# Kernel tuning notes

Hardware: AMD Instinct MI355X
Metric: run time of the kernel (lower is better)

## Reference

```python
import jax, jax.numpy as jnp
import numpy as np
import math

BATCH, LEN, HID, STATE = 16, 4096, 512, 128
DT_MIN, DT_MAX = 1e-3, 0.1
STEP_RESCALE = 1.0
CONJ_SYM = True


def setup_inputs() -> dict:
    key = jax.random.key(0)
    ks = jax.random.split(key, 7)
    inputs = jax.random.normal(ks[0], (BATCH, LEN, HID), jnp.float32)
    # stable continuous-time eigenvalues: negative real part
    lambda_real = -0.5 * jnp.abs(jax.random.normal(ks[1], (STATE,), jnp.float32)) - 1e-3
    lambda_imag = jnp.pi * jax.random.normal(ks[2], (STATE,), jnp.float32)
    B = jax.random.normal(ks[3], (STATE, HID, 2), jnp.float32) * (1.0 / math.sqrt(HID))
    C = jax.random.normal(ks[4], (HID, STATE, 2), jnp.float32) * (1.0 / math.sqrt(STATE))
    D = jax.random.normal(ks[5], (HID,), jnp.float32)
    u = jax.random.uniform(ks[6], (STATE, 1), jnp.float32)
    log_step = u * (math.log(DT_MAX) - math.log(DT_MIN)) + math.log(DT_MIN)
    return dict(inputs=inputs, lambda_real=lambda_real, lambda_imag=lambda_imag,
                B=B, C=C, D=D, log_step=log_step)


def _s5_forward(inputs, lambda_real, lambda_imag, B, C, D, log_step):
    # complex diagonal state matrix (P,)
    lam = (lambda_real + 1j * lambda_imag).astype(jnp.complex64)
    step = STEP_RESCALE * jnp.exp(log_step[:, 0])          # (P,)
    lambda_bar = jnp.exp(lam * step.astype(jnp.complex64))  # ZOH discretization, (P,)
    B_c = (B[..., 0] + 1j * B[..., 1]).astype(jnp.complex64)  # (P, H)
    C_c = (C[..., 0] + 1j * C[..., 1]).astype(jnp.complex64)  # (H, P)
    # ZOH input matrix: B_bar = (lambda_bar - 1) / lambda * B
    b_bar = ((lambda_bar - 1.0) / lam)[:, None] * B_c          # (P, H)
    # per-timestep driving term: (L, B, P)
    bu = jnp.einsum('blh,ph->lbp', inputs.astype(jnp.complex64), b_bar)
    L = inputs.shape[1]
    a = jnp.broadcast_to(lambda_bar[None, None, :], (L, 1, STATE))  # constant decay per step

    def combine(e1, e2):
        a1, b1 = e1
        a2, b2 = e2
        return (a2 * a1, a2 * b1 + b2)

    # parallel (Blelchoch-style) scan of x_t = lambda_bar * x_{t-1} + bu_t
    _, states = jax.lax.associative_scan(combine, (a, bu))      # states: (L, B, P)
    y = jnp.einsum('lbp,hp->blh', states, C_c)                  # (B, L, H) complex
    out = 2.0 * y.real if CONJ_SYM else y.real
    return out + D * inputs


def reference(inputs, lambda_real, lambda_imag, B, C, D, log_step):
    return _s5_forward(inputs, lambda_real, lambda_imag, B, C, D, log_step)
```

## Files before the change

### kernel.cpp

```cpp
#include <hip/hip_runtime.h>
#include <math.h>

#define B_   16
#define L_   4096
#define H_   512
#define P_   128
#define M_   (B_*L_)
#define N2_  (2*P_)

typedef __attribute__((ext_vector_type(8))) short bf16x8;
typedef __attribute__((ext_vector_type(8))) unsigned short u16x8;
typedef __attribute__((ext_vector_type(4))) float f32x4;

__device__ __forceinline__ unsigned short f2bf(float x) {
    unsigned u = __float_as_uint(x);
    return (unsigned short)((u + 0x7FFFu + ((u >> 16) & 1u)) >> 16);
}
__device__ __forceinline__ float bf2f(unsigned short s) {
    return __uint_as_float(((unsigned)s) << 16);
}

__device__ __forceinline__ void gload16(const void* g, void* l) {
    __builtin_amdgcn_global_load_lds(
        (const __attribute__((address_space(1))) void*)g,
        (__attribute__((address_space(3))) void*)l,
        16, 0, 0);
}


__global__ void precompA(const float* __restrict__ lr, const float* __restrict__ li,
                         const float* __restrict__ lstep,
                         float* __restrict__ abar_r, float* __restrict__ abar_i,
                         float* __restrict__ coef_r, float* __restrict__ coef_i) {
    int p = threadIdx.x;
    if (p >= P_) return;
    double lrd = (double)lr[p], lid = (double)li[p];
    double step = exp((double)lstep[p]);
    double ea = exp(lrd * step);
    double abr = ea * cos(lid * step), abi = ea * sin(lid * step);
    abar_r[p] = (float)abr; abar_i[p] = (float)abi;
    double nr = abr - 1.0, ni = abi;
    double den = lrd*lrd + lid*lid;
    coef_r[p] = (float)((nr*lrd + ni*lid) / den);
    coef_i[p] = (float)((ni*lrd - nr*lid) / den);
}

__global__ void precompBT(const float* __restrict__ Bin,
                          const float* __restrict__ coef_r, const float* __restrict__ coef_i,
                          unsigned short* __restrict__ BTh) {
    int idx = blockIdx.x * 256 + threadIdx.x;
    if (idx >= N2_*H_) return;
    int n = idx >> 9, k = idx & 511;
    int p = n & (P_-1);
    float br = Bin[(p*H_ + k)*2 + 0], bi = Bin[(p*H_ + k)*2 + 1];
    float cr = coef_r[p], ci = coef_i[p];
    float v = (n < P_) ? (cr*br - ci*bi) : (cr*bi + ci*br);
    BTh[idx] = f2bf(v);
}

__global__ void precompCM(const float* __restrict__ Cin,
                          unsigned short* __restrict__ CMh) {
    int idx = blockIdx.x * 256 + threadIdx.x;
    if (idx >= H_*N2_) return;
    int n = idx >> 8, k = idx & 255;
    float v;
    if (k < P_) v =  2.0f * Cin[(n*P_ + k)*2 + 0];
    else        v = -2.0f * Cin[(n*P_ + (k-P_))*2 + 1];
    CMh[idx] = f2bf(v);
}


template<int KSTEPS>
__global__ __launch_bounds__(256) void gemm1f(
        const float* __restrict__ A,
        const unsigned short* __restrict__ Bm,
        unsigned short* __restrict__ bu) {
    constexpr int K = KSTEPS * 32;
    __shared__ float Asf[128 * 32];
    __shared__ unsigned short Bs[128 * 32];

    int t = threadIdx.x;
    int nx = gridDim.x;
    int flat = blockIdx.x + nx * blockIdx.y;
    int per  = (nx * gridDim.y) >> 3;
    int nid  = (flat & 7) * per + (flat >> 3);
    int n0 = (nid & (nx - 1)) * 128;
    int m0 = (nid / nx) * 128;

    int lane = t & 63;
    int w    = t >> 6;
    int wr = w >> 1, wc = w & 1;
    int lr = lane & 15, lg = lane >> 4;

    int arow = t >> 3, ach = t & 7;
    int asw  = ach ^ (arow & 7);
    const float* gA = A + (size_t)(m0 + arow) * K + asw * 4;
    int brow = t >> 2, bch = t & 3;
    const unsigned short* gB = Bm + (size_t)(n0 + brow) * K + bch * 8;
    int bbase = w * 512;

    f32x4 acc[4][4] = {};

    for (int ks = 0; ks < KSTEPS; ++ks) {
        int k0 = ks * 32;
        __syncthreads();
#pragma unroll
        for (int i = 0; i < 4; ++i)
            gload16(gA + (size_t)(32 * i) * K + k0, &Asf[i * 1024 + w * 256]);
        gload16(gB + k0,                   &Bs[bbase]);
        gload16(gB + (size_t)64 * K + k0,  &Bs[2048 + bbase]);
        __syncthreads();

        bf16x8 af[4], bf[4];
#pragma unroll
        for (int f = 0; f < 4; ++f) {
            int rA = wr * 64 + f * 16 + lr;
            int c0 = ((2 * lg) ^ (rA & 7)) * 4;
            int c1 = ((2 * lg + 1) ^ (rA & 7)) * 4;
            float4 a0 = *(const float4*)&Asf[rA * 32 + c0];
            float4 a1 = *(const float4*)&Asf[rA * 32 + c1];
            u16x8 h;
            h[0] = f2bf(a0.x); h[1] = f2bf(a0.y); h[2] = f2bf(a0.z); h[3] = f2bf(a0.w);
            h[4] = f2bf(a1.x); h[5] = f2bf(a1.y); h[6] = f2bf(a1.z); h[7] = f2bf(a1.w);
            af[f] = *(bf16x8*)&h;
            int rB = wc * 64 + f * 16 + lr;
            bf[f] = *(const bf16x8*)&Bs[rB * 32 + lg * 8];
        }
#pragma unroll
        for (int fn = 0; fn < 4; ++fn)
#pragma unroll
            for (int fm = 0; fm < 4; ++fm)
                acc[fn][fm] = __builtin_amdgcn_mfma_f32_16x16x32_bf16(bf[fn], af[fm], acc[fn][fm], 0, 0, 0);
    }

#pragma unroll
    for (int fn = 0; fn < 4; ++fn)
#pragma unroll
        for (int fm = 0; fm < 4; ++fm) {
            int m = m0 + wr * 64 + fm * 16 + lr;
            int n = n0 + wc * 64 + fn * 16 + lg * 4;
            ushort4 o;
            o.x = f2bf(acc[fn][fm][0]); o.y = f2bf(acc[fn][fm][1]);
            o.z = f2bf(acc[fn][fm][2]); o.w = f2bf(acc[fn][fm][3]);
            *(ushort4*)&bu[(size_t)m * N2_ + n] = o;
        }
}


template<int KSTEPS, bool HASD>
__global__ __launch_bounds__(256) void gemm_m97(
        const unsigned short* __restrict__ A,
        const unsigned short* __restrict__ Bm,
        float* __restrict__ Cout, int N,
        const float* __restrict__ Din, const float* __restrict__ Dv) {
    constexpr int K = KSTEPS * 32;
    __shared__ unsigned short As[128 * 32];
    __shared__ unsigned short Bs[128 * 32];

    int t = threadIdx.x;
    int nx = gridDim.x;
    int flat = blockIdx.x + nx * blockIdx.y;
    int per  = (nx * gridDim.y) >> 3;
    int nid  = (flat & 7) * per + (flat >> 3);
    int n0 = (nid & (nx - 1)) * 128;
    int m0 = (nid / nx) * 128;

    int lane = t & 63;
    int w    = t >> 6;
    int wr = w >> 1, wc = w & 1;
    int lr = lane & 15, lg = lane >> 4;

    int srow = t >> 2;
    int sq   = t & 3;
    const unsigned short* gA = A  + (size_t)(m0 + srow) * K + sq * 8;
    const unsigned short* gB = Bm + (size_t)(n0 + srow) * K + sq * 8;
    int ldsb = w * 512;

    f32x4 acc[4][4] = {};

    for (int ks = 0; ks < KSTEPS; ++ks) {
        int k0 = ks * 32;
        __syncthreads();
        gload16(gA + k0,                  As + ldsb);
        gload16(gA + (size_t)64 * K + k0, As + 2048 + ldsb);
        gload16(gB + k0,                  Bs + ldsb);
        gload16(gB + (size_t)64 * K + k0, Bs + 2048 + ldsb);
        __syncthreads();

        bf16x8 af[4], bf[4];
#pragma unroll
        for (int f = 0; f < 4; ++f) {
            af[f] = *(const bf16x8*)&As[(wr * 64 + f * 16 + lr) * 32 + lg * 8];
            bf[f] = *(const bf16x8*)&Bs[(wc * 64 + f * 16 + lr) * 32 + lg * 8];
        }
#pragma unroll
        for (int fn = 0; fn < 4; ++fn)
#pragma unroll
            for (int fm = 0; fm < 4; ++fm)
                acc[fn][fm] = __builtin_amdgcn_mfma_f32_16x16x32_bf16(bf[fn], af[fm], acc[fn][fm], 0, 0, 0);
    }

#pragma unroll
    for (int fn = 0; fn < 4; ++fn)
#pragma unroll
        for (int fm = 0; fm < 4; ++fm) {
            int m = m0 + wr * 64 + fm * 16 + lr;
            int n = n0 + wc * 64 + fn * 16 + lg * 4;
            float4 v = make_float4(acc[fn][fm][0], acc[fn][fm][1], acc[fn][fm][2], acc[fn][fm][3]);
            if (HASD) {
                float4 di = *(const float4*)&Din[(size_t)m * N + n];
                float4 dv = *(const float4*)&Dv[n];
                v.x += dv.x * di.x; v.y += dv.y * di.y;
                v.z += dv.z * di.z; v.w += dv.w * di.w;
            }
            *(float4*)&Cout[(size_t)m * N + n] = v;
        }
}


__global__ __launch_bounds__(256) void scan_carry(const unsigned short* __restrict__ bu,
        const float* __restrict__ ar_, const float* __restrict__ ai_,
        float* __restrict__ carr) {
    __shared__ float lds[64][256];
    int t = threadIdx.x;
    int c = blockIdx.x, b = blockIdx.y;
    size_t base = ((size_t)(b*L_ + c*256)) * N2_;
    float ar = 0.f, ai = 0.f, xr = 0.f, xi = 0.f;
    if (t < 128) { ar = ar_[t]; ai = ai_[t]; }
    for (int s = 0; s < 4; s++) {
        __syncthreads();
        const unsigned short* g = bu + base + (size_t)s * 64 * N2_;
#pragma unroll
        for (int it = 0; it < 8; it++) {
            int flat = it * 2048 + t * 8;
            u16x8 v = *(const u16x8*)&g[flat];
            float4 x0 = make_float4(bf2f(v[0]), bf2f(v[1]), bf2f(v[2]), bf2f(v[3]));
            float4 x1 = make_float4(bf2f(v[4]), bf2f(v[5]), bf2f(v[6]), bf2f(v[7]));
            *(float4*)&lds[0][flat]     = x0;
            *(float4*)&lds[0][flat + 4] = x1;
        }
        __syncthreads();
        if (t < 128) {
            for (int i = 0; i < 64; i++) {
                float br = lds[i][t], bi = lds[i][t + 128];
                float nr = ar*xr - ai*xi + br;
                float ni = ar*xi + ai*xr + bi;
                xr = nr; xi = ni;
            }
        }
    }
    if (t < 128) {
        size_t o = ((size_t)(b*16 + c)) * N2_;
        carr[o + t] = xr; carr[o + t + 128] = xi;
    }
}

__global__ void scan_chunks(const float* __restrict__ carr, float* __restrict__ pre,
                            const float* __restrict__ ar_, const float* __restrict__ ai_) {
    int id = blockIdx.x * 256 + threadIdx.x;
    if (id >= B_ * P_) return;
    int b = id >> 7, p = id & (P_-1);
    float mr = ar_[p], mi = ai_[p];
#pragma unroll
    for (int s = 0; s < 8; s++) { float tr = mr*mr - mi*mi; mi = 2.f*mr*mi; mr = tr; }
    float xr = 0.f, xi = 0.f;
    for (int c = 0; c < 16; c++) {
        size_t o = ((size_t)(b*16 + c)) * N2_;
        pre[o + p] = xr; pre[o + p + 128] = xi;
        float cr = carr[o + p], ci = carr[o + p + 128];
        float nr = mr*xr - mi*xi + cr;
        float ni = mr*xi + mi*xr + ci;
        xr = nr; xi = ni;
    }
}

__global__ __launch_bounds__(256) void scan_apply(const unsigned short* __restrict__ bu,
        const float* __restrict__ ar_, const float* __restrict__ ai_,
        const float* __restrict__ pre, unsigned short* __restrict__ states_h) {
    __shared__ float lds[64][256];
    int t = threadIdx.x;
    int c = blockIdx.x, b = blockIdx.y;
    size_t base = ((size_t)(b*L_ + c*256)) * N2_;
    float ar = 0.f, ai = 0.f, xr = 0.f, xi = 0.f;
    if (t < 128) {
        ar = ar_[t]; ai = ai_[t];
        size_t o = ((size_t)(b*16 + c)) * N2_;
        xr = pre[o + t]; xi = pre[o + t + 128];
    }
    for (int s = 0; s < 4; s++) {
        __syncthreads();
        const unsigned short* g = bu + base + (size_t)s * 64 * N2_;
#pragma unroll
        for (int it = 0; it < 8; it++) {
            int flat = it * 2048 + t * 8;
            u16x8 v = *(const u16x8*)&g[flat];
            float4 x0 = make_float4(bf2f(v[0]), bf2f(v[1]), bf2f(v[2]), bf2f(v[3]));
            float4 x1 = make_float4(bf2f(v[4]), bf2f(v[5]), bf2f(v[6]), bf2f(v[7]));
            *(float4*)&lds[0][flat]     = x0;
            *(float4*)&lds[0][flat + 4] = x1;
        }
        __syncthreads();
        if (t < 128) {
            for (int i = 0; i < 64; i++) {
                float br = lds[i][t], bi = lds[i][t + 128];
                float nr = ar*xr - ai*xi + br;
                float ni = ar*xi + ai*xr + bi;
                xr = nr; xi = ni;
                lds[i][t] = xr; lds[i][t + 128] = xi;
            }
        }
        __syncthreads();
        unsigned short* o = states_h + base + (size_t)s * 64 * N2_;
#pragma unroll
        for (int it = 0; it < 8; it++) {
            int flat = it * 2048 + t * 8;
            float4 v0 = *(const float4*)&lds[0][flat];
            float4 v1 = *(const float4*)&lds[0][flat + 4];
            u16x8 ov;
            ov[0] = f2bf(v0.x); ov[1] = f2bf(v0.y); ov[2] = f2bf(v0.z); ov[3] = f2bf(v0.w);
            ov[4] = f2bf(v1.x); ov[5] = f2bf(v1.y); ov[6] = f2bf(v1.z); ov[7] = f2bf(v1.w);
            *(u16x8*)&o[flat] = ov;
        }
    }
}


extern "C" void kernel_launch(void* const* d_in, const int* in_sizes, int n_in,
                              void* d_out, int out_size, void* d_ws, size_t ws_size,
                              hipStream_t stream) {
    const float* inputs = (const float*)d_in[0];
    const float* lr     = (const float*)d_in[1];
    const float* li     = (const float*)d_in[2];
    const float* Bin    = (const float*)d_in[3];
    const float* Cin    = (const float*)d_in[4];
    const float* Dv     = (const float*)d_in[5];
    const float* lstep  = (const float*)d_in[6];
    float* out = (float*)d_out;

    unsigned short* bu = (unsigned short*)d_out;

    float* ws     = (float*)d_ws;
    float* abar_r = ws;
    float* abar_i = ws + 128;
    float* coef_r = ws + 256;
    float* coef_i = ws + 384;
    float* carr   = ws + 512;
    float* pre    = ws + 66048;
    unsigned short* BTh = (unsigned short*)(ws + 131584);
    unsigned short* CMh = BTh + N2_*H_;
    unsigned short* states_h = CMh + H_*N2_;

    hipLaunchKernelGGL(precompA, dim3(1), dim3(128), 0, stream,
                       lr, li, lstep, abar_r, abar_i, coef_r, coef_i);
    hipLaunchKernelGGL(precompBT, dim3((N2_*H_)/256), dim3(256), 0, stream,
                       Bin, coef_r, coef_i, BTh);
    hipLaunchKernelGGL(precompCM, dim3((H_*N2_)/256), dim3(256), 0, stream,
                       Cin, CMh);
    hipLaunchKernelGGL((gemm1f<16>), dim3(N2_/128, M_/128), dim3(256), 0, stream,
                       inputs, BTh, bu);
    hipLaunchKernelGGL(scan_carry, dim3(16, B_), dim3(256), 0, stream,
                       bu, abar_r, abar_i, carr);
    hipLaunchKernelGGL(scan_chunks, dim3(8), dim3(256), 0, stream,
                       carr, pre, abar_r, abar_i);
    hipLaunchKernelGGL(scan_apply, dim3(16, B_), dim3(256), 0, stream,
                       bu, abar_r, abar_i, pre, states_h);
    hipLaunchKernelGGL((gemm_m97<8, true>), dim3(H_/128, M_/128), dim3(256), 0, stream,
                       states_h, CMh, out, H_, inputs, Dv);
}
```

Baseline: 155.1 us.

## Triple-buffer LDS tiles with async prefetch in both GEMM kernels

Both GEMM kernels now use three LDS buffers and prefetch tiles two K-steps ahead with global_load_lds. Each step waits only on the current tile via vmcnt and a single barrier, where before it used two __syncthreads per step. The goal is to overlap global-to-LDS loads with MFMA compute and to raise wave priority during the MFMA block. This triples LDS use per block, which may lower occupancy, and the hand-set vmcnt counts depend on the exact number of loads per stage.

```diff
diff --git a/kernel.cpp b/kernel.cpp
--- a/kernel.cpp
+++ b/kernel.cpp
@@ -76,8 +76,8 @@
         const unsigned short* __restrict__ Bm,
         unsigned short* __restrict__ bu) {
     constexpr int K = KSTEPS * 32;
-    __shared__ float Asf[128 * 32];
-    __shared__ unsigned short Bs[128 * 32];
+    __shared__ float Asf[3][128 * 32];
+    __shared__ unsigned short Bs[3][128 * 32];
 
     int t = threadIdx.x;
     int nx = gridDim.x;
@@ -101,15 +101,33 @@
 
     f32x4 acc[4][4] = {};
 
+#define STAGE1(BUF, KS0)                                                     \
+    {                                                                        \
+        int k0_ = (KS0) * 32;                                                \
+        _Pragma("unroll")                                                    \
+        for (int i = 0; i < 4; ++i)                                          \
+            gload16(gA + (size_t)(32 * i) * K + k0_,                         \
+                    &Asf[BUF][i * 1024 + w * 256]);                          \
+        gload16(gB + k0_,                  &Bs[BUF][bbase]);                 \
+        gload16(gB + (size_t)64 * K + k0_, &Bs[BUF][2048 + bbase]);          \
+    }
+
+    STAGE1(0, 0);
+    STAGE1(1, 1);
+
+#pragma unroll
     for (int ks = 0; ks < KSTEPS; ++ks) {
-        int k0 = ks * 32;
-        __syncthreads();
-#pragma unroll
-        for (int i = 0; i < 4; ++i)
-            gload16(gA + (size_t)(32 * i) * K + k0, &Asf[i * 1024 + w * 256]);
-        gload16(gB + k0,                   &Bs[bbase]);
-        gload16(gB + (size_t)64 * K + k0,  &Bs[2048 + bbase]);
-        __syncthreads();
+        int cur = ks % 3;
+        if (ks + 1 < KSTEPS) {
+            asm volatile("s_waitcnt vmcnt(6)" ::: "memory");
+        } else {
+            asm volatile("s_waitcnt vmcnt(0)" ::: "memory");
+        }
+        __builtin_amdgcn_sched_barrier(0);
+        __builtin_amdgcn_s_barrier();
+        __builtin_amdgcn_sched_barrier(0);
+        if (ks + 2 < KSTEPS)
+            STAGE1((ks + 2) % 3, ks + 2);
 
         bf16x8 af[4], bf[4];
 #pragma unroll
@@ -117,21 +135,24 @@
             int rA = wr * 64 + f * 16 + lr;
             int c0 = ((2 * lg) ^ (rA & 7)) * 4;
             int c1 = ((2 * lg + 1) ^ (rA & 7)) * 4;
-            float4 a0 = *(const float4*)&Asf[rA * 32 + c0];
-            float4 a1 = *(const float4*)&Asf[rA * 32 + c1];
+            float4 a0 = *(const float4*)&Asf[cur][rA * 32 + c0];
+            float4 a1 = *(const float4*)&Asf[cur][rA * 32 + c1];
             u16x8 h;
             h[0] = f2bf(a0.x); h[1] = f2bf(a0.y); h[2] = f2bf(a0.z); h[3] = f2bf(a0.w);
             h[4] = f2bf(a1.x); h[5] = f2bf(a1.y); h[6] = f2bf(a1.z); h[7] = f2bf(a1.w);
             af[f] = *(bf16x8*)&h;
             int rB = wc * 64 + f * 16 + lr;
-            bf[f] = *(const bf16x8*)&Bs[rB * 32 + lg * 8];
-        }
+            bf[f] = *(const bf16x8*)&Bs[cur][rB * 32 + lg * 8];
+        }
+        __builtin_amdgcn_s_setprio(1);
 #pragma unroll
         for (int fn = 0; fn < 4; ++fn)
 #pragma unroll
             for (int fm = 0; fm < 4; ++fm)
                 acc[fn][fm] = __builtin_amdgcn_mfma_f32_16x16x32_bf16(bf[fn], af[fm], acc[fn][fm], 0, 0, 0);
-    }
+        __builtin_amdgcn_s_setprio(0);
+    }
+#undef STAGE1
 
 #pragma unroll
     for (int fn = 0; fn < 4; ++fn)
@@ -154,8 +175,8 @@
         float* __restrict__ Cout, int N,
         const float* __restrict__ Din, const float* __restrict__ Dv) {
     constexpr int K = KSTEPS * 32;
-    __shared__ unsigned short As[128 * 32];
-    __shared__ unsigned short Bs[128 * 32];
+    __shared__ unsigned short As[3][128 * 32];
+    __shared__ unsigned short Bs[3][128 * 32];
 
     int t = threadIdx.x;
     int nx = gridDim.x;
@@ -178,27 +199,47 @@
 
     f32x4 acc[4][4] = {};
 
+#define STAGE2(BUF, KS0)                                                     \
+    {                                                                        \
+        int k0_ = (KS0) * 32;                                                \
+        gload16(gA + k0_,                  &As[BUF][ldsb]);                  \
+        gload16(gA + (size_t)64 * K + k0_, &As[BUF][2048 + ldsb]);           \
+        gload16(gB + k0_,                  &Bs[BUF][ldsb]);                  \
+        gload16(gB + (size_t)64 * K + k0_, &Bs[BUF][2048 + ldsb]);           \
+    }
+
+    STAGE2(0, 0);
+    STAGE2(1, 1);
+
+#pragma unroll
     for (int ks = 0; ks < KSTEPS; ++ks) {
-        int k0 = ks * 32;
-        __syncthreads();
-        gload16(gA + k0,                  As + ldsb);
-        gload16(gA + (size_t)64 * K + k0, As + 2048 + ldsb);
-        gload16(gB + k0,                  Bs + ldsb);
-        gload16(gB + (size_t)64 * K + k0, Bs + 2048 + ldsb);
-        __syncthreads();
+        int cur = ks % 3;
+        if (ks + 1 < KSTEPS) {
+            asm volatile("s_waitcnt vmcnt(4)" ::: "memory");
+        } else {
+            asm volatile("s_waitcnt vmcnt(0)" ::: "memory");
+        }
+        __builtin_amdgcn_sched_barrier(0);
+        __builtin_amdgcn_s_barrier();
+        __builtin_amdgcn_sched_barrier(0);
+        if (ks + 2 < KSTEPS)
+            STAGE2((ks + 2) % 3, ks + 2);
 
         bf16x8 af[4], bf[4];
 #pragma unroll
         for (int f = 0; f < 4; ++f) {
-            af[f] = *(const bf16x8*)&As[(wr * 64 + f * 16 + lr) * 32 + lg * 8];
-            bf[f] = *(const bf16x8*)&Bs[(wc * 64 + f * 16 + lr) * 32 + lg * 8];
-        }
+            af[f] = *(const bf16x8*)&As[cur][(wr * 64 + f * 16 + lr) * 32 + lg * 8];
+            bf[f] = *(const bf16x8*)&Bs[cur][(wc * 64 + f * 16 + lr) * 32 + lg * 8];
+        }
+        __builtin_amdgcn_s_setprio(1);
 #pragma unroll
         for (int fn = 0; fn < 4; ++fn)
 #pragma unroll
             for (int fm = 0; fm < 4; ++fm)
                 acc[fn][fm] = __builtin_amdgcn_mfma_f32_16x16x32_bf16(bf[fn], af[fm], acc[fn][fm], 0, 0, 0);
-    }
+        __builtin_amdgcn_s_setprio(0);
+    }
+#undef STAGE2
 
 #pragma unroll
     for (int fn = 0; fn < 4; ++fn)
```

Result: slower. 175.3 us (+13.0%).

## Retile input projection GEMM to 64x256 tiles covering full N

Applied to the files above, without the earlier changes.

The first GEMM now uses 64-row by 256-column tiles, so each block covers the entire 2P output width. Before, it used 128x128 tiles with two N-blocks per M-row. The fp32 input activations are therefore read from global memory once instead of twice, and converted to bf16 once instead of twice. In exchange, each block reloads the full B matrix, and the grid doubles to twice as many smaller-M blocks.

```diff
diff --git a/kernel.cpp b/kernel.cpp
--- a/kernel.cpp
+++ b/kernel.cpp
@@ -76,28 +76,23 @@
         const unsigned short* __restrict__ Bm,
         unsigned short* __restrict__ bu) {
     constexpr int K = KSTEPS * 32;
-    __shared__ float Asf[128 * 32];
-    __shared__ unsigned short Bs[128 * 32];
+    __shared__ float Asf[64 * 32];
+    __shared__ unsigned short Bs[256 * 32];
 
     int t = threadIdx.x;
-    int nx = gridDim.x;
-    int flat = blockIdx.x + nx * blockIdx.y;
-    int per  = (nx * gridDim.y) >> 3;
-    int nid  = (flat & 7) * per + (flat >> 3);
-    int n0 = (nid & (nx - 1)) * 128;
-    int m0 = (nid / nx) * 128;
+    int g = blockIdx.x;
+    int nid = (g & 7) * (gridDim.x >> 3) + (g >> 3);
+    int m0 = nid * 64;
 
     int lane = t & 63;
     int w    = t >> 6;
-    int wr = w >> 1, wc = w & 1;
     int lr = lane & 15, lg = lane >> 4;
 
     int arow = t >> 3, ach = t & 7;
     int asw  = ach ^ (arow & 7);
     const float* gA = A + (size_t)(m0 + arow) * K + asw * 4;
-    int brow = t >> 2, bch = t & 3;
-    const unsigned short* gB = Bm + (size_t)(n0 + brow) * K + bch * 8;
-    int bbase = w * 512;
+    int brow = t >> 2;
+    const unsigned short* gB = Bm + (size_t)brow * K + (t & 3) * 8;
 
     f32x4 acc[4][4] = {};
 
@@ -105,16 +100,17 @@
         int k0 = ks * 32;
         __syncthreads();
 #pragma unroll
-        for (int i = 0; i < 4; ++i)
+        for (int i = 0; i < 2; ++i)
             gload16(gA + (size_t)(32 * i) * K + k0, &Asf[i * 1024 + w * 256]);
-        gload16(gB + k0,                   &Bs[bbase]);
-        gload16(gB + (size_t)64 * K + k0,  &Bs[2048 + bbase]);
+#pragma unroll
+        for (int j = 0; j < 4; ++j)
+            gload16(gB + (size_t)(64 * j) * K + k0, &Bs[j * 2048 + w * 512]);
         __syncthreads();
 
         bf16x8 af[4], bf[4];
 #pragma unroll
         for (int f = 0; f < 4; ++f) {
-            int rA = wr * 64 + f * 16 + lr;
+            int rA = f * 16 + lr;
             int c0 = ((2 * lg) ^ (rA & 7)) * 4;
             int c1 = ((2 * lg + 1) ^ (rA & 7)) * 4;
             float4 a0 = *(const float4*)&Asf[rA * 32 + c0];
@@ -123,7 +119,7 @@
             h[0] = f2bf(a0.x); h[1] = f2bf(a0.y); h[2] = f2bf(a0.z); h[3] = f2bf(a0.w);
             h[4] = f2bf(a1.x); h[5] = f2bf(a1.y); h[6] = f2bf(a1.z); h[7] = f2bf(a1.w);
             af[f] = *(bf16x8*)&h;
-            int rB = wc * 64 + f * 16 + lr;
+            int rB = w * 64 + f * 16 + lr;
             bf[f] = *(const bf16x8*)&Bs[rB * 32 + lg * 8];
         }
 #pragma unroll
@@ -137,8 +133,8 @@
     for (int fn = 0; fn < 4; ++fn)
 #pragma unroll
         for (int fm = 0; fm < 4; ++fm) {
-            int m = m0 + wr * 64 + fm * 16 + lr;
-            int n = n0 + wc * 64 + fn * 16 + lg * 4;
+            int m = m0 + fm * 16 + lr;
+            int n = w * 64 + fn * 16 + lg * 4;
             ushort4 o;
             o.x = f2bf(acc[fn][fm][0]); o.y = f2bf(acc[fn][fm][1]);
             o.z = f2bf(acc[fn][fm][2]); o.w = f2bf(acc[fn][fm][3]);
@@ -356,7 +352,7 @@
                        Bin, coef_r, coef_i, BTh);
     hipLaunchKernelGGL(precompCM, dim3((H_*N2_)/256), dim3(256), 0, stream,
                        Cin, CMh);
-    hipLaunchKernelGGL((gemm1f<16>), dim3(N2_/128, M_/128), dim3(256), 0, stream,
+    hipLaunchKernelGGL((gemm1f<16>), dim3(M_/64), dim3(256), 0, stream,
                        inputs, BTh, bu);
     hipLaunchKernelGGL(scan_carry, dim3(16, B_), dim3(256), 0, stream,
                        bu, abar_r, abar_i, carr);
```

Result: no change. 154.5 us (-0.4%).
